# Performance work log

Measured on AMD Instinct MI355X. Metric: run time of the kernel, lower is better.

Reference implementation:

```python
import jax, jax.numpy as jnp
import numpy as np

B, L, P = 64, 256, 32
LANE_DIM, EMBED, DEPTH, HEADS = 2, 128, 4, 8
MLP = 4 * EMBED
HD = EMBED // HEADS
MASK_RATIO, ELIG = 0.5, 5


def _glorot(key, shape):
    lim = float(np.sqrt(6.0 / (shape[-2] + shape[-1])))
    return jax.random.uniform(key, shape, jnp.float32, -lim, lim)


def setup_inputs() -> dict:
    key = jax.random.key(0)
    ks = jax.random.split(key, 24)
    lane_positions = jax.random.normal(ks[0], (B, L, P, LANE_DIM), jnp.float32)
    lane_centers = jax.random.normal(ks[1], (B, L, LANE_DIM), jnp.float32)
    lane_angles = jax.random.normal(ks[2], (B, L), jnp.float32)
    # ragged padding + random masking, precomputed (externalizes torch randperm loop)
    rng = np.random.default_rng(0)
    pad = rng.random((B, L, P)) < 0.2  # True = padding
    valid = ~pad
    num_valid = valid.sum(-1)                      # (B,L)
    eligible = num_valid > ELIG
    num_mask = (num_valid * MASK_RATIO).astype(np.int32)  # trunc == .int()
    scores = np.where(valid, rng.random((B, L, P)), 2.0)
    rank = scores.argsort(-1).argsort(-1)          # rank of each valid point
    sel = (rank < num_mask[..., None]) & valid & eligible[..., None]
    inp = {
        'lane_positions': lane_positions,
        'lane_centers': lane_centers,
        'lane_angles': lane_angles,
        'lane_padding_mask': jnp.asarray(pad),
        'sel_mask': jnp.asarray(sel),
        'Wp': _glorot(ks[3], (LANE_DIM, EMBED)), 'bp': jnp.zeros((EMBED,)),
        'Wpe1': _glorot(ks[4], (4, EMBED)), 'bpe1': jnp.zeros((EMBED,)),
        'Wpe2': _glorot(ks[5], (EMBED, EMBED)), 'bpe2': jnp.zeros((EMBED,)),
        'lane_type': 0.02 * jax.random.normal(ks[6], (EMBED,), jnp.float32),
        'mask_token': 0.02 * jax.random.normal(ks[7], (EMBED,), jnp.float32),
        'Wqkv': _glorot(ks[8], (DEPTH, EMBED, 3 * EMBED)), 'bqkv': jnp.zeros((DEPTH, 3 * EMBED)),
        'Wo': _glorot(ks[9], (DEPTH, EMBED, EMBED)), 'bo': jnp.zeros((DEPTH, EMBED)),
        'ln1_s': jnp.ones((DEPTH, EMBED)), 'ln1_b': jnp.zeros((DEPTH, EMBED)),
        'Wm1': _glorot(ks[10], (DEPTH, EMBED, MLP)), 'bm1': jnp.zeros((DEPTH, MLP)),
        'Wm2': _glorot(ks[11], (DEPTH, MLP, EMBED)), 'bm2': jnp.zeros((DEPTH, EMBED)),
        'ln2_s': jnp.ones((DEPTH, EMBED)), 'ln2_b': jnp.zeros((DEPTH, EMBED)),
        'lnf_s': jnp.ones((EMBED,)), 'lnf_b': jnp.zeros((EMBED,)),
        'Wd1': _glorot(ks[12], (EMBED, MLP)), 'bd1': jnp.zeros((MLP,)),
        'Wd2': _glorot(ks[13], (MLP, LANE_DIM)), 'bd2': jnp.zeros((LANE_DIM,)),
    }
    return inp


def _ln(x, s, b):
    m = jnp.mean(x, -1, keepdims=True)
    v = jnp.var(x, -1, keepdims=True)
    return (x - m) * jax.lax.rsqrt(v + 1e-5) * s + b


def _forward(lane_positions, lane_centers, lane_angles, Wp, bp, Wpe1, bpe1,
             Wpe2, bpe2, lane_type, mask_token, Wqkv, bqkv, Wo, bo, ln1_s,
             ln1_b, Wm1, bm1, Wm2, bm2, ln2_s, ln2_b, lnf_s, lnf_b, Wd1, bd1,
             Wd2, bd2, sel_mask):
    lane_norm = lane_positions - lane_centers[:, :, None, :]      # (B,L,P,2)
    feat = lane_norm @ Wp + bp                                    # (B,L,P,E)
    pos_feat = jnp.concatenate([lane_centers,
                                jnp.cos(lane_angles)[..., None],
                                jnp.sin(lane_angles)[..., None]], -1)  # (B,L,4)
    pe = jax.nn.gelu(pos_feat @ Wpe1 + bpe1, approximate=False) @ Wpe2 + bpe2
    tok = feat + pe[:, :, None, :] + lane_type
    tok = jnp.where(sel_mask[..., None], mask_token, tok)
    x = tok.reshape(B * L, P, EMBED)
    scale = 1.0 / np.sqrt(HD).astype(np.float32)
    for i in range(DEPTH):  # SpaNet: pre-LN transformer encoder over points
        h = _ln(x, ln1_s[i], ln1_b[i])
        q, k, v = jnp.split(h @ Wqkv[i] + bqkv[i], 3, axis=-1)
        q = q.reshape(B * L, P, HEADS, HD)
        k = k.reshape(B * L, P, HEADS, HD)
        v = v.reshape(B * L, P, HEADS, HD)
        att = jax.nn.softmax(jnp.einsum('nqhd,nkhd->nhqk', q, k) * scale, -1)
        o = jnp.einsum('nhqk,nkhd->nqhd', att, v).reshape(B * L, P, EMBED)
        x = x + o @ Wo[i] + bo[i]
        h = _ln(x, ln2_s[i], ln2_b[i])
        x = x + jax.nn.gelu(h @ Wm1[i] + bm1[i], approximate=False) @ Wm2[i] + bm2[i]
    x = _ln(x, lnf_s, lnf_b)
    y = (jax.nn.relu(x @ Wd1 + bd1) @ Wd2 + bd2).reshape(B, L, P, LANE_DIM)
    selc = sel_mask[..., None].astype(y.dtype)
    sq = (y - lane_norm) ** 2
    loss = jnp.sum(sq * selc) / jnp.maximum(jnp.sum(selc) * LANE_DIM, 1.0)
    return loss, y


def reference(lane_positions, lane_centers, lane_angles, lane_padding_mask,
              sel_mask, Wp, bp, Wpe1, bpe1, Wpe2, bpe2, lane_type, mask_token,
              Wqkv, bqkv, Wo, bo, ln1_s, ln1_b, Wm1, bm1, Wm2, bm2, ln2_s,
              ln2_b, lnf_s, lnf_b, Wd1, bd1, Wd2, bd2):
    del lane_padding_mask  # already folded into sel_mask during setup
    return _forward(lane_positions, lane_centers, lane_angles, Wp, bp, Wpe1,
                    bpe1, Wpe2, bpe2, lane_type, mask_token, Wqkv, bqkv, Wo,
                    bo, ln1_s, ln1_b, Wm1, bm1, Wm2, bm2, ln2_s, ln2_b, lnf_s,
                    lnf_b, Wd1, bd1, Wd2, bd2, sel_mask)
```

## Files before the change

kernel.cpp:

```cpp
#include <hip/hip_runtime.h>


#define NP 32
#define NE 128
#define NSEQ (64 * 256)
#define NMLP 512
#define NDEPTH 4
#define LST 132
#define HBS 136
#define H1C 264

#define QKV_W_OFF 0
#define O_W_OFF   196608
#define M1_W_OFF  262144
#define M2_W_OFF  524288
#define D1_W_OFF  786432
#define W_TOTAL   851968
#define WS_NEED   (64 + (size_t)W_TOTAL * 2)

typedef unsigned short u16;
typedef unsigned int u32;
typedef __attribute__((ext_vector_type(8))) short bf16x8;
typedef __attribute__((ext_vector_type(4))) float f32x4;
#define MFMA16 __builtin_amdgcn_mfma_f32_16x16x32_bf16

__device__ __forceinline__ float b2f(u16 u) {
  union { u32 i; float f; } v; v.i = ((u32)u) << 16; return v.f;
}
__device__ __forceinline__ u16 f2b(float f) {
  union { float f; u32 i; } v; v.f = f;
  u32 x = v.i;
  x += 0x7fffu + ((x >> 16) & 1u);
  return (u16)(x >> 16);
}
__device__ __forceinline__ u32 pk2(float lo, float hi) {
  return (u32)f2b(lo) | ((u32)f2b(hi) << 16);
}
__device__ __forceinline__ float gelu_f(float x) {
  return 0.5f * x * (1.0f + erff(x * 0.7071067811865475f));
}

struct Args {
  const float *pos, *ctr, *ang;
  const int *sel;
  const float *Wp, *bp, *Wpe1, *bpe1, *Wpe2, *bpe2, *ltype, *mtok;
  const float *Wqkv, *bqkv, *Wo, *bo, *ln1s, *ln1b, *Wm1, *bm1, *Wm2, *bm2;
  const float *ln2s, *ln2b, *lnfs, *lnfb, *Wd1, *bd1, *Wd2, *bd2;
  float* out;
  float* wsf;
  int* wsi;
};

__global__ void pack_w(const float* __restrict__ src, u16* __restrict__ dst,
                       int K, int N, int L) {
  int id = blockIdx.x * 256 + threadIdx.x;
  int KT = K >> 5, NT = N >> 4;
  int total = L * NT * KT * 64;
  if (id >= total) return;
  int lane = id & 63;
  int rest = id >> 6;
  int kt = rest % KT;
  int rest2 = rest / KT;
  int nt = rest2 % NT;
  int l = rest2 / NT;
  const float* s = src + (size_t)l * K * N + (size_t)(kt * 32 + (lane >> 4) * 8) * N
                 + nt * 16 + (lane & 15);
  u16 tmp[8];
#pragma unroll
  for (int j = 0; j < 8; ++j) tmp[j] = f2b(s[(size_t)j * N]);
  ((uint4*)dst)[id] = *(const uint4*)tmp;
}

template <int NTW>
__device__ __forceinline__ void gemm_kt4(const u16* __restrict__ hA, int SA,
                                         const u16* __restrict__ B, int w,
                                         int lane, f32x4 (&acc)[NTW][2]) {
  int ar = lane & 15, ac = (lane >> 4) * 8;
  bf16x8 af[8];
#pragma unroll
  for (int kb = 0; kb < 4; ++kb) {
    af[kb]     = *(const bf16x8*)(hA + ar * SA + kb * 32 + ac);
    af[kb + 4] = *(const bf16x8*)(hA + (ar + 16) * SA + kb * 32 + ac);
  }
#pragma unroll
  for (int i = 0; i < NTW; ++i) {
    int nt = w + 4 * i;
    const u16* Bp = B + (size_t)nt * 2048 + lane * 8;
    f32x4 z = {0.f, 0.f, 0.f, 0.f};
    acc[i][0] = z; acc[i][1] = z;
#pragma unroll
    for (int kb = 0; kb < 4; ++kb) {
      bf16x8 b = *(const bf16x8*)(Bp + kb * 512);
      acc[i][0] = MFMA16(af[kb], b, acc[i][0], 0, 0, 0);
      acc[i][1] = MFMA16(af[kb + 4], b, acc[i][1], 0, 0, 0);
    }
  }
}

__device__ __forceinline__ void gemm_kt8_acc(const u16* __restrict__ hA,
                                             const u16* __restrict__ B, int ktoff,
                                             int w, int lane, f32x4 (&acc)[2][2]) {
  int ar = lane & 15, ac = (lane >> 4) * 8;
#pragma unroll
  for (int ktl = 0; ktl < 8; ++ktl) {
    bf16x8 a0 = *(const bf16x8*)(hA + ar * H1C + ktl * 32 + ac);
    bf16x8 a1 = *(const bf16x8*)(hA + (ar + 16) * H1C + ktl * 32 + ac);
#pragma unroll
    for (int i = 0; i < 2; ++i) {
      int nt = w + 4 * i;
      bf16x8 b = *(const bf16x8*)(B + (size_t)nt * 8192 + (size_t)(ktoff + ktl) * 512 + lane * 8);
      acc[i][0] = MFMA16(a0, b, acc[i][0], 0, 0, 0);
      acc[i][1] = MFMA16(a1, b, acc[i][1], 0, 0, 0);
    }
  }
}

__device__ __forceinline__ void layer_norm_bf(const float* __restrict__ src,
                                              u16* __restrict__ dst,
                                              const float* gam, const float* bet,
                                              int t, float* mrow, float* vrow) {
  int p = t >> 3, j0 = (t & 7) * 16;
  const float* row = src + p * LST + j0;
  float sum = 0.f, sq = 0.f;
#pragma unroll
  for (int k = 0; k < 16; ++k) { float v = row[k]; sum += v; sq += v * v; }
#pragma unroll
  for (int o = 1; o < 8; o <<= 1) { sum += __shfl_xor(sum, o); sq += __shfl_xor(sq, o); }
  if ((t & 7) == 0) {
    float m = sum * 0.0078125f;
    mrow[p] = m;
    vrow[p] = sq * 0.0078125f - m * m;
  }
  __syncthreads();
  float m = mrow[p], rs = rsqrtf(vrow[p] + 1e-5f);
  u32 wb[8];
#pragma unroll
  for (int k8 = 0; k8 < 4; ++k8) {
    float4 v = ((const float4*)row)[k8];
    float4 g = ((const float4*)(gam + j0))[k8];
    float4 b = ((const float4*)(bet + j0))[k8];
    wb[k8 * 2]     = pk2((v.x - m) * rs * g.x + b.x, (v.y - m) * rs * g.y + b.y);
    wb[k8 * 2 + 1] = pk2((v.z - m) * rs * g.z + b.z, (v.w - m) * rs * g.w + b.w);
  }
  uint4* dp = (uint4*)(dst + p * HBS + j0);
  dp[0] = make_uint4(wb[0], wb[1], wb[2], wb[3]);
  dp[1] = make_uint4(wb[4], wb[5], wb[6], wb[7]);
  __syncthreads();
}

__global__ __launch_bounds__(256, 3) void mrm_main_mfma(Args a, const u16* __restrict__ wsW) {
  __shared__ float xs[32 * LST];
  __shared__ u16 hbf[32 * HBS];
  __shared__ __align__(16) u32 uni4[6144];
  __shared__ float mrow[32], vrow[32];
  __shared__ int selv[32];
  __shared__ float lacc;

  u16* qbuf = (u16*)uni4;
  u16* kbuf = qbuf + 4096;
  u16* vbuf = kbuf + 4096;
  u32* vbuf_w = (u32*)vbuf;
  u16* h1c  = (u16*)uni4;
  float* wd2s = (float*)uni4 + 4224;
  float* tvec = (float*)uni4;
  float* pvec = (float*)uni4 + 128;

  const int s = blockIdx.x;
  const int t = threadIdx.x;
  const int w = t >> 6, lane = t & 63;
  const int cr = lane & 15, rq = (lane >> 4) * 4;
  const int rg = t >> 5, cg = t & 31, r0 = rg * 4, c0 = cg * 4;

  if (t == 0) lacc = 0.f;
  if (t < 32) selv[t] = a.sel[s * NP + t];

  const float cx = a.ctr[s * 2 + 0];
  const float cy = a.ctr[s * 2 + 1];
  const float an = a.ang[s];
  const float ca = cosf(an), sa = sinf(an);

  if (t < 128) {
    float accp = a.bpe1[t] + cx * a.Wpe1[t] + cy * a.Wpe1[128 + t]
               + ca * a.Wpe1[256 + t] + sa * a.Wpe1[384 + t];
    tvec[t] = gelu_f(accp);
  }
  __syncthreads();
  if (t < 128) {
    float accp = a.bpe2[t];
    for (int e = 0; e < 128; ++e) accp += tvec[e] * a.Wpe2[e * 128 + t];
    pvec[t] = accp;
  }
  __syncthreads();

  {
    float4 w0v = *(const float4*)(a.Wp + c0);
    float4 w1v = *(const float4*)(a.Wp + NE + c0);
    float4 bpv = *(const float4*)(a.bp + c0);
    float4 ltv = *(const float4*)(a.ltype + c0);
    float4 mtv = *(const float4*)(a.mtok + c0);
    float a0 = bpv.x + pvec[c0 + 0] + ltv.x;
    float a1 = bpv.y + pvec[c0 + 1] + ltv.y;
    float a2 = bpv.z + pvec[c0 + 2] + ltv.z;
    float a3 = bpv.w + pvec[c0 + 3] + ltv.w;
#pragma unroll
    for (int rr = 0; rr < 4; ++rr) {
      int p = r0 + rr;
      float px = a.pos[(s * NP + p) * 2 + 0] - cx;
      float py = a.pos[(s * NP + p) * 2 + 1] - cy;
      bool mk = selv[p] != 0;
      float4 o;
      o.x = mk ? mtv.x : (px * w0v.x + py * w1v.x + a0);
      o.y = mk ? mtv.y : (px * w0v.y + py * w1v.y + a1);
      o.z = mk ? mtv.z : (px * w0v.z + py * w1v.z + a2);
      o.w = mk ? mtv.w : (px * w0v.w + py * w1v.w + a3);
      *(float4*)&xs[p * LST + c0] = o;
    }
  }
  __syncthreads();

  for (int li = 0; li < NDEPTH; ++li) {
    const u16* qkvW = wsW + QKV_W_OFF + li * 49152;
    const u16* oW   = wsW + O_W_OFF   + li * 16384;
    const u16* m1W  = wsW + M1_W_OFF  + li * 65536;
    const u16* m2W  = wsW + M2_W_OFF  + li * 65536;
    const float* bqkv_i = a.bqkv + li * 384;
    const float* bo_i   = a.bo + li * NE;
    const float* bm1_i  = a.bm1 + li * NMLP;
    const float* bm2_i  = a.bm2 + li * NE;

    layer_norm_bf(xs, hbf, a.ln1s + li * NE, a.ln1b + li * NE, t, mrow, vrow);

    {
      f32x4 acc[6][2];
      gemm_kt4<6>(hbf, HBS, qkvW, w, lane, acc);
#pragma unroll
      for (int i = 0; i < 6; ++i) {
        int nt = w + 4 * i;
        int n = nt * 16 + cr;
        float bias = bqkv_i[n];
        float v0[4], v1[4];
#pragma unroll
        for (int j = 0; j < 4; ++j) { v0[j] = acc[i][0][j] + bias; v1[j] = acc[i][1][j] + bias; }
        if (i < 2) {
          u16* qb = qbuf + nt * 512 + cr;
#pragma unroll
          for (int j = 0; j < 4; ++j) {
            qb[(rq + j) * 16]      = f2b(v0[j] * 0.25f);
            qb[(rq + j + 16) * 16] = f2b(v1[j] * 0.25f);
          }
        } else if (i < 4) {
          u16* kb = kbuf + (nt - 8) * 512 + cr;
#pragma unroll
          for (int j = 0; j < 4; ++j) {
            kb[(rq + j) * 16]      = f2b(v0[j]);
            kb[(rq + j + 16) * 16] = f2b(v1[j]);
          }
        } else {
          u32* vb = vbuf_w + (nt - 16) * 256 + cr * 16 + (rq >> 1);
          vb[0] = pk2(v0[0], v0[1]);
          vb[1] = pk2(v0[2], v0[3]);
          vb[8] = pk2(v1[0], v1[1]);
          vb[9] = pk2(v1[2], v1[3]);
        }
      }
    }
    __syncthreads();

    {
      const int l15 = lane & 15, gl = lane >> 4;
      const int bpa_base = (l15 + ((gl & 1) << 5)) << 2;
      const f32x4 z = {0.f, 0.f, 0.f, 0.f};
#pragma unroll
      for (int hi = 0; hi < 2; ++hi) {
        const int h = 2 * w + hi;
        const u16* qb = qbuf + h * 512;
        const u16* kb = kbuf + h * 512;
        bf16x8 vf = *(const bf16x8*)(vbuf + h * 512 + l15 * 32 + gl * 8);
        bf16x8 kf0 = {}, kf1 = {};
        if (gl < 2) {
          kf0 = *(const bf16x8*)(kb + l15 * 16 + gl * 8);
          kf1 = *(const bf16x8*)(kb + (16 + l15) * 16 + gl * 8);
        }
#pragma unroll
        for (int qt = 0; qt < 2; ++qt) {
          bf16x8 qf = {};
          if (gl < 2) qf = *(const bf16x8*)(qb + (qt * 16 + l15) * 16 + gl * 8);
          f32x4 s0 = MFMA16(kf0, qf, z, 0, 0, 0);
          f32x4 s1 = MFMA16(kf1, qf, z, 0, 0, 0);
          float mx = fmaxf(fmaxf(fmaxf(s0[0], s0[1]), fmaxf(s0[2], s0[3])),
                           fmaxf(fmaxf(s1[0], s1[1]), fmaxf(s1[2], s1[3])));
          mx = fmaxf(mx, __shfl_xor(mx, 16));
          mx = fmaxf(mx, __shfl_xor(mx, 32));
          float p0 = __expf(s0[0] - mx), p1 = __expf(s0[1] - mx);
          float p2 = __expf(s0[2] - mx), p3 = __expf(s0[3] - mx);
          float p4 = __expf(s1[0] - mx), p5 = __expf(s1[1] - mx);
          float p6 = __expf(s1[2] - mx), p7 = __expf(s1[3] - mx);
          float sum = ((p0 + p1) + (p2 + p3)) + ((p4 + p5) + (p6 + p7));
          sum += __shfl_xor(sum, 16);
          sum += __shfl_xor(sum, 32);
          float inv = 1.f / sum;
          u32 pw0 = pk2(p0 * inv, p1 * inv), pw1 = pk2(p2 * inv, p3 * inv);
          u32 pw2 = pk2(p4 * inv, p5 * inv), pw3 = pk2(p6 * inv, p7 * inv);
          union { u32 uw[4]; bf16x8 v; } pa;
#pragma unroll
          for (int ww = 0; ww < 4; ++ww) {
            int addr = bpa_base + ((ww >> 1) << 6);
            u32 lo = __builtin_amdgcn_ds_bpermute(addr, (int)((ww & 1) ? pw1 : pw0));
            u32 hi2 = __builtin_amdgcn_ds_bpermute(addr, (int)((ww & 1) ? pw3 : pw2));
            pa.uw[ww] = (gl < 2) ? lo : hi2;
          }
          f32x4 o = MFMA16(pa.v, vf, z, 0, 0, 0);
#pragma unroll
          for (int j = 0; j < 4; ++j)
            hbf[(qt * 16 + gl * 4 + j) * HBS + h * 16 + l15] = f2b(o[j]);
        }
      }
    }
    __syncthreads();

    {
      f32x4 acc[2][2];
      gemm_kt4<2>(hbf, HBS, oW, w, lane, acc);
#pragma unroll
      for (int i = 0; i < 2; ++i) {
        int n = (w + 4 * i) * 16 + cr;
        float bias = bo_i[n];
#pragma unroll
        for (int j = 0; j < 4; ++j) {
          xs[(rq + j) * LST + n]      += acc[i][0][j] + bias;
          xs[(rq + j + 16) * LST + n] += acc[i][1][j] + bias;
        }
      }
    }
    __syncthreads();

    layer_norm_bf(xs, hbf, a.ln2s + li * NE, a.ln2b + li * NE, t, mrow, vrow);

    {
      f32x4 acc2[2][2];
      f32x4 z = {0.f, 0.f, 0.f, 0.f};
      acc2[0][0] = z; acc2[0][1] = z; acc2[1][0] = z; acc2[1][1] = z;
#pragma unroll
      for (int ch = 0; ch < 2; ++ch) {
        {
          f32x4 acc[4][2];
          gemm_kt4<4>(hbf, HBS, m1W + ch * 32768, w, lane, acc);
#pragma unroll
          for (int i = 0; i < 4; ++i) {
            int nl = (w + 4 * i) * 16 + cr;
            float bias = bm1_i[ch * 256 + nl];
#pragma unroll
            for (int j = 0; j < 4; ++j) {
              h1c[(rq + j) * H1C + nl]      = f2b(gelu_f(acc[i][0][j] + bias));
              h1c[(rq + j + 16) * H1C + nl] = f2b(gelu_f(acc[i][1][j] + bias));
            }
          }
        }
        __syncthreads();
        gemm_kt8_acc(h1c, m2W, ch * 8, w, lane, acc2);
        __syncthreads();
      }
      {
        f32x4* a2 = &acc2[0][0];
#pragma unroll
        for (int i = 0; i < 2; ++i) {
          int n = (w + 4 * i) * 16 + cr;
          float bias = bm2_i[n];
#pragma unroll
          for (int j = 0; j < 4; ++j) {
            xs[(rq + j) * LST + n]      += acc2[i][0][j] + bias;
            xs[(rq + j + 16) * LST + n] += acc2[i][1][j] + bias;
          }
        }
        (void)a2;
      }
    }
    __syncthreads();
  }

  layer_norm_bf(xs, hbf, a.lnfs, a.lnfb, t, mrow, vrow);

  for (int i = t; i < 1024; i += 256) wd2s[i] = a.Wd2[i];

  float yacc = 0.f;
  const int pdec = t >> 3, dd2 = (t >> 2) & 1, q4 = t & 3;
#pragma unroll
  for (int ch = 0; ch < 2; ++ch) {
    {
      f32x4 acc[4][2];
      gemm_kt4<4>(hbf, HBS, wsW + D1_W_OFF + ch * 32768, w, lane, acc);
#pragma unroll
      for (int i = 0; i < 4; ++i) {
        int nl = (w + 4 * i) * 16 + cr;
        float bias = a.bd1[ch * 256 + nl];
#pragma unroll
        for (int j = 0; j < 4; ++j) {
          h1c[(rq + j) * H1C + nl]      = f2b(fmaxf(acc[i][0][j] + bias, 0.f));
          h1c[(rq + j + 16) * H1C + nl] = f2b(fmaxf(acc[i][1][j] + bias, 0.f));
        }
      }
    }
    __syncthreads();
    {
      const u16* hrow = h1c + pdec * H1C + q4 * 64;
      const float* wp = wd2s + (ch * 256 + q4 * 64) * 2 + dd2;
#pragma unroll
      for (int k8 = 0; k8 < 8; ++k8) {
        bf16x8 hv = *(const bf16x8*)(hrow + k8 * 8);
#pragma unroll
        for (int jj = 0; jj < 8; ++jj)
          yacc += b2f((u16)hv[jj]) * wp[(k8 * 8 + jj) * 2];
      }
    }
    __syncthreads();
  }

  {
    yacc += __shfl_xor(yacc, 1);
    yacc += __shfl_xor(yacc, 2);
    if (q4 == 0) {
      float y = yacc + a.bd2[dd2];
      a.out[1 + (s * NP + pdec) * 2 + dd2] = y;
      float lnm = a.pos[(s * NP + pdec) * 2 + dd2] - (dd2 ? cy : cx);
      float d = y - lnm;
      if (selv[pdec] != 0) atomicAdd(&lacc, d * d);
    }
  }
  __syncthreads();
  if (t == 0) {
    atomicAdd(a.wsf, lacc);
    int cnt = 0;
#pragma unroll
    for (int p = 0; p < NP; ++p) cnt += (selv[p] != 0) ? 1 : 0;
    atomicAdd(a.wsi, cnt);
  }
}

__device__ __forceinline__ void mm128(const float* __restrict__ src,
                                      const float* __restrict__ W, int ldw,
                                      int r0, int cabs, float acc[4][4]) {
#pragma unroll 4
  for (int k = 0; k < NE; ++k) {
    float4 wv = *(const float4*)(W + k * ldw + cabs);
#pragma unroll
    for (int rr = 0; rr < 4; ++rr) {
      float sv = src[(r0 + rr) * LST + k];
      acc[rr][0] += sv * wv.x; acc[rr][1] += sv * wv.y;
      acc[rr][2] += sv * wv.z; acc[rr][3] += sv * wv.w;
    }
  }
}

__device__ __forceinline__ void layer_norm(const float* __restrict__ src,
                                           float* __restrict__ dst,
                                           const float* gam, const float* bet,
                                           int t, float* mrow, float* vrow) {
  {
    int p = t >> 3, j = t & 7;
    const float* row = src + p * LST + j * 16;
    float sum = 0.f, sq = 0.f;
#pragma unroll
    for (int k2 = 0; k2 < 16; ++k2) { float v = row[k2]; sum += v; sq += v * v; }
#pragma unroll
    for (int o = 1; o < 8; o <<= 1) { sum += __shfl_xor(sum, o); sq += __shfl_xor(sq, o); }
    if (j == 0) {
      float m = sum * 0.0078125f;
      mrow[p] = m;
      vrow[p] = sq * 0.0078125f - m * m;
    }
  }
  __syncthreads();
  {
    int rg = t >> 5, cg = t & 31, r0 = rg * 4, c0 = cg * 4;
    float4 gv = *(const float4*)(gam + c0);
    float4 bv = *(const float4*)(bet + c0);
#pragma unroll
    for (int rr = 0; rr < 4; ++rr) {
      int r = r0 + rr;
      float m = mrow[r], rs = rsqrtf(vrow[r] + 1e-5f);
      float4 v = *(const float4*)&src[r * LST + c0];
      float4 o;
      o.x = (v.x - m) * rs * gv.x + bv.x;
      o.y = (v.y - m) * rs * gv.y + bv.y;
      o.z = (v.z - m) * rs * gv.z + bv.z;
      o.w = (v.w - m) * rs * gv.w + bv.w;
      *(float4*)&dst[r * LST + c0] = o;
    }
  }
  __syncthreads();
}

__global__ __launch_bounds__(256, 2) void mrm_main_valu(Args a) {
  __shared__ float xs[32 * LST];
  __shared__ float hs[32 * LST];
  __shared__ float ts[32 * LST];
  __shared__ float qs[32 * 17];
  __shared__ float ks2[32 * 17];
  __shared__ float vs[32 * 17];
  __shared__ float ss[32 * 33];
  __shared__ float tvec[128];
  __shared__ float pvec[128];
  __shared__ float mrow[32], vrow[32], srow[32];
  __shared__ int selv[32];

  const int s = blockIdx.x;
  const int t = threadIdx.x;
  const int rg = t >> 5, cg = t & 31, r0 = rg * 4, c0 = cg * 4;

  if (t < 32) selv[t] = a.sel[s * NP + t];

  const float cx = a.ctr[s * 2 + 0];
  const float cy = a.ctr[s * 2 + 1];
  const float an = a.ang[s];
  const float ca = cosf(an), sa = sinf(an);

  if (t < 128) {
    float accp = a.bpe1[t] + cx * a.Wpe1[t] + cy * a.Wpe1[128 + t]
               + ca * a.Wpe1[256 + t] + sa * a.Wpe1[384 + t];
    tvec[t] = gelu_f(accp);
  }
  __syncthreads();
  if (t < 128) {
    float accp = a.bpe2[t];
    for (int e = 0; e < 128; ++e) accp += tvec[e] * a.Wpe2[e * 128 + t];
    pvec[t] = accp;
  }
  __syncthreads();

  {
    float4 w0v = *(const float4*)(a.Wp + c0);
    float4 w1v = *(const float4*)(a.Wp + NE + c0);
    float4 bpv = *(const float4*)(a.bp + c0);
    float4 ltv = *(const float4*)(a.ltype + c0);
    float4 mtv = *(const float4*)(a.mtok + c0);
    float a0 = bpv.x + pvec[c0 + 0] + ltv.x;
    float a1 = bpv.y + pvec[c0 + 1] + ltv.y;
    float a2 = bpv.z + pvec[c0 + 2] + ltv.z;
    float a3 = bpv.w + pvec[c0 + 3] + ltv.w;
#pragma unroll
    for (int rr = 0; rr < 4; ++rr) {
      int p = r0 + rr;
      float px = a.pos[(s * NP + p) * 2 + 0] - cx;
      float py = a.pos[(s * NP + p) * 2 + 1] - cy;
      bool mk = selv[p] != 0;
      float4 o;
      o.x = mk ? mtv.x : (px * w0v.x + py * w1v.x + a0);
      o.y = mk ? mtv.y : (px * w0v.y + py * w1v.y + a1);
      o.z = mk ? mtv.z : (px * w0v.z + py * w1v.z + a2);
      o.w = mk ? mtv.w : (px * w0v.w + py * w1v.w + a3);
      *(float4*)&xs[p * LST + c0] = o;
    }
  }
  __syncthreads();

  const int dd = t & 15, ph = t >> 4;

  for (int li = 0; li < NDEPTH; ++li) {
    const float* Wqkv_i = a.Wqkv + li * NE * 3 * NE;
    const float* bqkv_i = a.bqkv + li * 3 * NE;
    const float* Wo_i   = a.Wo   + li * NE * NE;
    const float* bo_i   = a.bo   + li * NE;
    const float* Wm1_i  = a.Wm1  + li * NE * NMLP;
    const float* bm1_i  = a.bm1  + li * NMLP;
    const float* Wm2_i  = a.Wm2  + li * NMLP * NE;
    const float* bm2_i  = a.bm2  + li * NE;

    layer_norm(xs, hs, a.ln1s + li * NE, a.ln1b + li * NE, t, mrow, vrow);

    for (int hh = 0; hh < 8; ++hh) {
      float aq0 = 0, aq1 = 0, ak0 = 0, ak1 = 0, av0 = 0, av1 = 0;
      const float* wcol = Wqkv_i + hh * 16 + dd;
#pragma unroll 4
      for (int k2 = 0; k2 < NE; ++k2) {
        const float* wr = wcol + k2 * (3 * NE);
        float wq = wr[0], wk = wr[NE], wv = wr[2 * NE];
        float h0 = hs[ph * LST + k2], h1 = hs[(ph + 16) * LST + k2];
        aq0 += h0 * wq; aq1 += h1 * wq;
        ak0 += h0 * wk; ak1 += h1 * wk;
        av0 += h0 * wv; av1 += h1 * wv;
      }
      {
        float bq = bqkv_i[hh * 16 + dd];
        float bk = bqkv_i[NE + hh * 16 + dd];
        float bv = bqkv_i[2 * NE + hh * 16 + dd];
        qs[ph * 17 + dd] = aq0 + bq;  qs[(ph + 16) * 17 + dd] = aq1 + bq;
        ks2[ph * 17 + dd] = ak0 + bk; ks2[(ph + 16) * 17 + dd] = ak1 + bk;
        vs[ph * 17 + dd] = av0 + bv;  vs[(ph + 16) * 17 + dd] = av1 + bv;
      }
      __syncthreads();
      {
        int pk = t & 31, pb = t >> 5;
#pragma unroll
        for (int ii = 0; ii < 4; ++ii) {
          int p = pb + 8 * ii;
          float acc = 0.f;
#pragma unroll
          for (int d2 = 0; d2 < 16; ++d2) acc += qs[p * 17 + d2] * ks2[pk * 17 + d2];
          ss[p * 33 + pk] = 0.25f * acc;
        }
      }
      __syncthreads();
      {
        int p = t >> 3, j = t & 7;
        float v0 = ss[p * 33 + j * 4 + 0], v1 = ss[p * 33 + j * 4 + 1];
        float v2 = ss[p * 33 + j * 4 + 2], v3 = ss[p * 33 + j * 4 + 3];
        float mx = fmaxf(fmaxf(v0, v1), fmaxf(v2, v3));
#pragma unroll
        for (int o = 1; o < 8; o <<= 1) mx = fmaxf(mx, __shfl_xor(mx, o));
        v0 = expf(v0 - mx); v1 = expf(v1 - mx); v2 = expf(v2 - mx); v3 = expf(v3 - mx);
        float sm = v0 + v1 + v2 + v3;
#pragma unroll
        for (int o = 1; o < 8; o <<= 1) sm += __shfl_xor(sm, o);
        ss[p * 33 + j * 4 + 0] = v0; ss[p * 33 + j * 4 + 1] = v1;
        ss[p * 33 + j * 4 + 2] = v2; ss[p * 33 + j * 4 + 3] = v3;
        if (j == 0) srow[p] = sm;
      }
      __syncthreads();
      {
        float o0 = 0.f, o1 = 0.f;
#pragma unroll
        for (int pk = 0; pk < 32; ++pk) {
          float vv = vs[pk * 17 + dd];
          o0 += ss[ph * 33 + pk] * vv;
          o1 += ss[(ph + 16) * 33 + pk] * vv;
        }
        ts[ph * LST + hh * 16 + dd] = o0 / srow[ph];
        ts[(ph + 16) * LST + hh * 16 + dd] = o1 / srow[ph + 16];
      }
      __syncthreads();
    }

    {
      float acc[4][4] = {};
      mm128(ts, Wo_i, NE, r0, c0, acc);
      float4 bv = *(const float4*)(bo_i + c0);
#pragma unroll
      for (int rr = 0; rr < 4; ++rr) {
        float4 v = *(float4*)&xs[(r0 + rr) * LST + c0];
        v.x += acc[rr][0] + bv.x; v.y += acc[rr][1] + bv.y;
        v.z += acc[rr][2] + bv.z; v.w += acc[rr][3] + bv.w;
        *(float4*)&xs[(r0 + rr) * LST + c0] = v;
      }
    }
    __syncthreads();

    layer_norm(xs, hs, a.ln2s + li * NE, a.ln2b + li * NE, t, mrow, vrow);

    {
      float acc2[4][4] = {};
      for (int ch = 0; ch < 4; ++ch) {
        float acc[4][4] = {};
        mm128(hs, Wm1_i, NMLP, r0, ch * 128 + c0, acc);
        float4 bv = *(const float4*)(bm1_i + ch * 128 + c0);
#pragma unroll
        for (int rr = 0; rr < 4; ++rr) {
          float4 o;
          o.x = gelu_f(acc[rr][0] + bv.x); o.y = gelu_f(acc[rr][1] + bv.y);
          o.z = gelu_f(acc[rr][2] + bv.z); o.w = gelu_f(acc[rr][3] + bv.w);
          *(float4*)&ts[(r0 + rr) * LST + c0] = o;
        }
        __syncthreads();
        mm128(ts, Wm2_i + ch * 128 * NE, NE, r0, c0, acc2);
        __syncthreads();
      }
      float4 bv = *(const float4*)(bm2_i + c0);
#pragma unroll
      for (int rr = 0; rr < 4; ++rr) {
        float4 v = *(float4*)&xs[(r0 + rr) * LST + c0];
        v.x += acc2[rr][0] + bv.x; v.y += acc2[rr][1] + bv.y;
        v.z += acc2[rr][2] + bv.z; v.w += acc2[rr][3] + bv.w;
        *(float4*)&xs[(r0 + rr) * LST + c0] = v;
      }
    }
    __syncthreads();
  }

  layer_norm(xs, hs, a.lnfs, a.lnfb, t, mrow, vrow);

  float yacc = 0.f;
  const int pdec = t >> 1, ddec = t & 1;
  for (int ch = 0; ch < 4; ++ch) {
    {
      float acc[4][4] = {};
      mm128(hs, a.Wd1, NMLP, r0, ch * 128 + c0, acc);
      float4 bv = *(const float4*)(a.bd1 + ch * 128 + c0);
#pragma unroll
      for (int rr = 0; rr < 4; ++rr) {
        float4 o;
        o.x = fmaxf(acc[rr][0] + bv.x, 0.f); o.y = fmaxf(acc[rr][1] + bv.y, 0.f);
        o.z = fmaxf(acc[rr][2] + bv.z, 0.f); o.w = fmaxf(acc[rr][3] + bv.w, 0.f);
        *(float4*)&ts[(r0 + rr) * LST + c0] = o;
      }
    }
    __syncthreads();
    if (t < 64) {
#pragma unroll 4
      for (int k2 = 0; k2 < 128; ++k2)
        yacc += ts[pdec * LST + k2] * a.Wd2[(ch * 128 + k2) * 2 + ddec];
    }
    __syncthreads();
  }

  if (t < 64) {
    float y = yacc + a.bd2[ddec];
    a.out[1 + (s * NP + pdec) * 2 + ddec] = y;
    float lnm = a.pos[(s * NP + pdec) * 2 + ddec] - (ddec ? cy : cx);
    float d = y - lnm;
    float part = (selv[pdec] != 0) ? d * d : 0.f;
#pragma unroll
    for (int o = 1; o < 64; o <<= 1) part += __shfl_xor(part, o);
    if (t == 0) {
      atomicAdd(a.wsf, part);
      int cnt = 0;
      for (int p = 0; p < NP; ++p) cnt += (selv[p] != 0) ? 1 : 0;
      atomicAdd(a.wsi, cnt);
    }
  }
}

__global__ void mrm_fin(const float* ws, float* out) {
  float num = ws[0];
  int cnt = ((const int*)ws)[1];
  float den = fmaxf((float)cnt * 2.0f, 1.0f);
  out[0] = num / den;
}

extern "C" void kernel_launch(void* const* d_in, const int* in_sizes, int n_in,
                              void* d_out, int out_size, void* d_ws, size_t ws_size,
                              hipStream_t stream) {
  (void)in_sizes; (void)n_in; (void)out_size;
  Args a;
  a.pos   = (const float*)d_in[0];
  a.ctr   = (const float*)d_in[1];
  a.ang   = (const float*)d_in[2];
  a.sel   = (const int*)d_in[4];
  a.Wp    = (const float*)d_in[5];
  a.bp    = (const float*)d_in[6];
  a.Wpe1  = (const float*)d_in[7];
  a.bpe1  = (const float*)d_in[8];
  a.Wpe2  = (const float*)d_in[9];
  a.bpe2  = (const float*)d_in[10];
  a.ltype = (const float*)d_in[11];
  a.mtok  = (const float*)d_in[12];
  a.Wqkv  = (const float*)d_in[13];
  a.bqkv  = (const float*)d_in[14];
  a.Wo    = (const float*)d_in[15];
  a.bo    = (const float*)d_in[16];
  a.ln1s  = (const float*)d_in[17];
  a.ln1b  = (const float*)d_in[18];
  a.Wm1   = (const float*)d_in[19];
  a.bm1   = (const float*)d_in[20];
  a.Wm2   = (const float*)d_in[21];
  a.bm2   = (const float*)d_in[22];
  a.ln2s  = (const float*)d_in[23];
  a.ln2b  = (const float*)d_in[24];
  a.lnfs  = (const float*)d_in[25];
  a.lnfb  = (const float*)d_in[26];
  a.Wd1   = (const float*)d_in[27];
  a.bd1   = (const float*)d_in[28];
  a.Wd2   = (const float*)d_in[29];
  a.bd2   = (const float*)d_in[30];
  a.out   = (float*)d_out;
  a.wsf   = (float*)d_ws;
  a.wsi   = ((int*)d_ws) + 1;

  hipMemsetAsync(d_ws, 0, 8, stream);
  if (ws_size >= WS_NEED) {
    u16* wsW = (u16*)((char*)d_ws + 64);
    pack_w<<<dim3(96),  dim3(256), 0, stream>>>(a.Wqkv, wsW + QKV_W_OFF, 128, 384, 4);
    pack_w<<<dim3(32),  dim3(256), 0, stream>>>(a.Wo,   wsW + O_W_OFF,   128, 128, 4);
    pack_w<<<dim3(128), dim3(256), 0, stream>>>(a.Wm1,  wsW + M1_W_OFF,  128, 512, 4);
    pack_w<<<dim3(128), dim3(256), 0, stream>>>(a.Wm2,  wsW + M2_W_OFF,  512, 128, 4);
    pack_w<<<dim3(32),  dim3(256), 0, stream>>>(a.Wd1,  wsW + D1_W_OFF,  128, 512, 1);
    mrm_main_mfma<<<dim3(NSEQ), dim3(256), 0, stream>>>(a, wsW);
  } else {
    mrm_main_valu<<<dim3(NSEQ), dim3(256), 0, stream>>>(a);
  }
  mrm_fin<<<dim3(1), dim3(1), 0, stream>>>((const float*)d_ws, (float*)d_out);
}
```

Baseline: 2.473 ms.

## Fold biases into MFMA accumulators, approximate GELU erf, pad V buffer, drop VALU fallback

Biases are now used as the initial MFMA accumulator values instead of being added in each epilogue. The 0.25 query scale is folded into the packed QKV weights and the query bias. The exact erff in GELU is replaced by an Abramowitz-Stegun polynomial with a fast reciprocal and exp, which cuts VALU work in the MLP at a small accuracy cost. The V buffer gets a padded row stride to reduce LDS bank conflicts, enlarging shared memory slightly. The VALU fallback path and the workspace size check are removed.

```diff
diff --git a/kernel.cpp b/kernel.cpp
--- a/kernel.cpp
+++ b/kernel.cpp
@@ -9,6 +9,7 @@
 #define LST 132
 #define HBS 136
 #define H1C 264
+#define VST 40
 
 #define QKV_W_OFF 0
 #define O_W_OFF   196608
@@ -36,8 +37,16 @@
 __device__ __forceinline__ u32 pk2(float lo, float hi) {
   return (u32)f2b(lo) | ((u32)f2b(hi) << 16);
 }
+
 __device__ __forceinline__ float gelu_f(float x) {
-  return 0.5f * x * (1.0f + erff(x * 0.7071067811865475f));
+  float z = fabsf(x) * 0.7071067811865476f;
+  float t = __builtin_amdgcn_rcpf(fmaf(z, 0.3275911f, 1.0f));
+  float poly = t * fmaf(t, fmaf(t, fmaf(t, fmaf(t, 1.061405429f, -1.453152027f),
+                        1.421413741f), -0.284496736f), 0.254829592f);
+  float e = __expf(-z * z);
+  float erf_abs = fmaf(-poly, e, 1.0f);
+  float erf = copysignf(erf_abs, x);
+  return 0.5f * x * (1.0f + erf);
 }
 
 struct Args {
@@ -52,7 +61,7 @@
 };
 
 __global__ void pack_w(const float* __restrict__ src, u16* __restrict__ dst,
-                       int K, int N, int L) {
+                       int K, int N, int L, int scaleN, float scale) {
   int id = blockIdx.x * 256 + threadIdx.x;
   int KT = K >> 5, NT = N >> 4;
   int total = L * NT * KT * 64;
@@ -63,18 +72,20 @@
   int rest2 = rest / KT;
   int nt = rest2 % NT;
   int l = rest2 / NT;
-  const float* s = src + (size_t)l * K * N + (size_t)(kt * 32 + (lane >> 4) * 8) * N
-                 + nt * 16 + (lane & 15);
+  int col = nt * 16 + (lane & 15);
+  float sc = (col < scaleN) ? scale : 1.0f;
+  const float* s = src + (size_t)l * K * N + (size_t)(kt * 32 + (lane >> 4) * 8) * N + col;
   u16 tmp[8];
 #pragma unroll
-  for (int j = 0; j < 8; ++j) tmp[j] = f2b(s[(size_t)j * N]);
+  for (int j = 0; j < 8; ++j) tmp[j] = f2b(s[(size_t)j * N] * sc);
   ((uint4*)dst)[id] = *(const uint4*)tmp;
 }
 
 template <int NTW>
-__device__ __forceinline__ void gemm_kt4(const u16* __restrict__ hA, int SA,
-                                         const u16* __restrict__ B, int w,
-                                         int lane, f32x4 (&acc)[NTW][2]) {
+__device__ __forceinline__ void gemm_kt4_b(const u16* __restrict__ hA, int SA,
+                                           const u16* __restrict__ B, int w,
+                                           int lane, const float* __restrict__ bias,
+                                           f32x4 (&acc)[NTW][2]) {
   int ar = lane & 15, ac = (lane >> 4) * 8;
   bf16x8 af[8];
 #pragma unroll
@@ -86,8 +97,9 @@
   for (int i = 0; i < NTW; ++i) {
     int nt = w + 4 * i;
     const u16* Bp = B + (size_t)nt * 2048 + lane * 8;
-    f32x4 z = {0.f, 0.f, 0.f, 0.f};
-    acc[i][0] = z; acc[i][1] = z;
+    float bb = bias[nt * 16 + ar];
+    f32x4 bi = {bb, bb, bb, bb};
+    acc[i][0] = bi; acc[i][1] = bi;
 #pragma unroll
     for (int kb = 0; kb < 4; ++kb) {
       bf16x8 b = *(const bf16x8*)(Bp + kb * 512);
@@ -139,8 +151,8 @@
     float4 v = ((const float4*)row)[k8];
     float4 g = ((const float4*)(gam + j0))[k8];
     float4 b = ((const float4*)(bet + j0))[k8];
-    wb[k8 * 2]     = pk2((v.x - m) * rs * g.x + b.x, (v.y - m) * rs * g.y + b.y);
-    wb[k8 * 2 + 1] = pk2((v.z - m) * rs * g.z + b.z, (v.w - m) * rs * g.w + b.w);
+    wb[k8 * 2]     = pk2(fmaf((v.x - m) * rs, g.x, b.x), fmaf((v.y - m) * rs, g.y, b.y));
+    wb[k8 * 2 + 1] = pk2(fmaf((v.z - m) * rs, g.z, b.z), fmaf((v.w - m) * rs, g.w, b.w));
   }
   uint4* dp = (uint4*)(dst + p * HBS + j0);
   dp[0] = make_uint4(wb[0], wb[1], wb[2], wb[3]);
@@ -151,7 +163,7 @@
 __global__ __launch_bounds__(256, 3) void mrm_main_mfma(Args a, const u16* __restrict__ wsW) {
   __shared__ float xs[32 * LST];
   __shared__ u16 hbf[32 * HBS];
-  __shared__ __align__(16) u32 uni4[6144];
+  __shared__ __align__(16) u32 uni4[6656];
   __shared__ float mrow[32], vrow[32];
   __shared__ int selv[32];
   __shared__ float lacc;
@@ -232,35 +244,53 @@
 
     {
       f32x4 acc[6][2];
-      gemm_kt4<6>(hbf, HBS, qkvW, w, lane, acc);
+      {
+        int ar = lane & 15, ac = (lane >> 4) * 8;
+        bf16x8 af[8];
+#pragma unroll
+        for (int kb = 0; kb < 4; ++kb) {
+          af[kb]     = *(const bf16x8*)(hbf + ar * HBS + kb * 32 + ac);
+          af[kb + 4] = *(const bf16x8*)(hbf + (ar + 16) * HBS + kb * 32 + ac);
+        }
+#pragma unroll
+        for (int i = 0; i < 6; ++i) {
+          int nt = w + 4 * i;
+          const u16* Bp = qkvW + (size_t)nt * 2048 + lane * 8;
+          float bb = bqkv_i[nt * 16 + ar];
+          if (i < 2) bb *= 0.25f;
+          f32x4 bi = {bb, bb, bb, bb};
+          acc[i][0] = bi; acc[i][1] = bi;
+#pragma unroll
+          for (int kb = 0; kb < 4; ++kb) {
+            bf16x8 b = *(const bf16x8*)(Bp + kb * 512);
+            acc[i][0] = MFMA16(af[kb], b, acc[i][0], 0, 0, 0);
+            acc[i][1] = MFMA16(af[kb + 4], b, acc[i][1], 0, 0, 0);
+          }
+        }
+      }
 #pragma unroll
       for (int i = 0; i < 6; ++i) {
         int nt = w + 4 * i;
-        int n = nt * 16 + cr;
-        float bias = bqkv_i[n];
-        float v0[4], v1[4];
-#pragma unroll
-        for (int j = 0; j < 4; ++j) { v0[j] = acc[i][0][j] + bias; v1[j] = acc[i][1][j] + bias; }
         if (i < 2) {
           u16* qb = qbuf + nt * 512 + cr;
 #pragma unroll
           for (int j = 0; j < 4; ++j) {
-            qb[(rq + j) * 16]      = f2b(v0[j] * 0.25f);
-            qb[(rq + j + 16) * 16] = f2b(v1[j] * 0.25f);
+            qb[(rq + j) * 16]      = f2b(acc[i][0][j]);
+            qb[(rq + j + 16) * 16] = f2b(acc[i][1][j]);
           }
         } else if (i < 4) {
           u16* kb = kbuf + (nt - 8) * 512 + cr;
 #pragma unroll
           for (int j = 0; j < 4; ++j) {
-            kb[(rq + j) * 16]      = f2b(v0[j]);
-            kb[(rq + j + 16) * 16] = f2b(v1[j]);
+            kb[(rq + j) * 16]      = f2b(acc[i][0][j]);
+            kb[(rq + j + 16) * 16] = f2b(acc[i][1][j]);
           }
         } else {
-          u32* vb = vbuf_w + (nt - 16) * 256 + cr * 16 + (rq >> 1);
-          vb[0] = pk2(v0[0], v0[1]);
-          vb[1] = pk2(v0[2], v0[3]);
-          vb[8] = pk2(v1[0], v1[1]);
-          vb[9] = pk2(v1[2], v1[3]);
+          u32* vb = vbuf_w + (nt - 16) * 320 + cr * 20 + (rq >> 1);
+          vb[0] = pk2(acc[i][0][0], acc[i][0][1]);
+          vb[1] = pk2(acc[i][0][2], acc[i][0][3]);
+          vb[8] = pk2(acc[i][1][0], acc[i][1][1]);
+          vb[9] = pk2(acc[i][1][2], acc[i][1][3]);
         }
       }
     }
@@ -275,7 +305,7 @@
         const int h = 2 * w + hi;
         const u16* qb = qbuf + h * 512;
         const u16* kb = kbuf + h * 512;
-        bf16x8 vf = *(const bf16x8*)(vbuf + h * 512 + l15 * 32 + gl * 8);
+        bf16x8 vf = *(const bf16x8*)(vbuf + h * 640 + l15 * VST + gl * 8);
         bf16x8 kf0 = {}, kf1 = {};
         if (gl < 2) {
           kf0 = *(const bf16x8*)(kb + l15 * 16 + gl * 8);
@@ -320,15 +350,14 @@
 
     {
       f32x4 acc[2][2];
-      gemm_kt4<2>(hbf, HBS, oW, w, lane, acc);
+      gemm_kt4_b<2>(hbf, HBS, oW, w, lane, bo_i, acc);
 #pragma unroll
       for (int i = 0; i < 2; ++i) {
         int n = (w + 4 * i) * 16 + cr;
-        float bias = bo_i[n];
 #pragma unroll
         for (int j = 0; j < 4; ++j) {
-          xs[(rq + j) * LST + n]      += acc[i][0][j] + bias;
-          xs[(rq + j + 16) * LST + n] += acc[i][1][j] + bias;
+          xs[(rq + j) * LST + n]      += acc[i][0][j];
+          xs[(rq + j + 16) * LST + n] += acc[i][1][j];
         }
       }
     }
@@ -338,21 +367,24 @@
 
     {
       f32x4 acc2[2][2];
-      f32x4 z = {0.f, 0.f, 0.f, 0.f};
-      acc2[0][0] = z; acc2[0][1] = z; acc2[1][0] = z; acc2[1][1] = z;
+#pragma unroll
+      for (int i = 0; i < 2; ++i) {
+        float bb = bm2_i[(w + 4 * i) * 16 + cr];
+        f32x4 bi = {bb, bb, bb, bb};
+        acc2[i][0] = bi; acc2[i][1] = bi;
+      }
 #pragma unroll
       for (int ch = 0; ch < 2; ++ch) {
         {
           f32x4 acc[4][2];
-          gemm_kt4<4>(hbf, HBS, m1W + ch * 32768, w, lane, acc);
+          gemm_kt4_b<4>(hbf, HBS, m1W + ch * 32768, w, lane, bm1_i + ch * 256, acc);
 #pragma unroll
           for (int i = 0; i < 4; ++i) {
             int nl = (w + 4 * i) * 16 + cr;
-            float bias = bm1_i[ch * 256 + nl];
 #pragma unroll
             for (int j = 0; j < 4; ++j) {
-              h1c[(rq + j) * H1C + nl]      = f2b(gelu_f(acc[i][0][j] + bias));
-              h1c[(rq + j + 16) * H1C + nl] = f2b(gelu_f(acc[i][1][j] + bias));
+              h1c[(rq + j) * H1C + nl]      = f2b(gelu_f(acc[i][0][j]));
+              h1c[(rq + j + 16) * H1C + nl] = f2b(gelu_f(acc[i][1][j]));
             }
           }
         }
@@ -360,19 +392,14 @@
         gemm_kt8_acc(h1c, m2W, ch * 8, w, lane, acc2);
         __syncthreads();
       }
-      {
-        f32x4* a2 = &acc2[0][0];
-#pragma unroll
-        for (int i = 0; i < 2; ++i) {
-          int n = (w + 4 * i) * 16 + cr;
-          float bias = bm2_i[n];
-#pragma unroll
-          for (int j = 0; j < 4; ++j) {
-            xs[(rq + j) * LST + n]      += acc2[i][0][j] + bias;
-            xs[(rq + j + 16) * LST + n] += acc2[i][1][j] + bias;
-          }
-        }
-        (void)a2;
+#pragma unroll
+      for (int i = 0; i < 2; ++i) {
+        int n = (w + 4 * i) * 16 + cr;
+#pragma unroll
+        for (int j = 0; j < 4; ++j) {
+          xs[(rq + j) * LST + n]      += acc2[i][0][j];
+          xs[(rq + j + 16) * LST + n] += acc2[i][1][j];
+        }
       }
     }
     __syncthreads();
@@ -388,15 +415,14 @@
   for (int ch = 0; ch < 2; ++ch) {
     {
       f32x4 acc[4][2];
-      gemm_kt4<4>(hbf, HBS, wsW + D1_W_OFF + ch * 32768, w, lane, acc);
+      gemm_kt4_b<4>(hbf, HBS, wsW + D1_W_OFF + ch * 32768, w, lane, a.bd1 + ch * 256, acc);
 #pragma unroll
       for (int i = 0; i < 4; ++i) {
         int nl = (w + 4 * i) * 16 + cr;
-        float bias = a.bd1[ch * 256 + nl];
 #pragma unroll
         for (int j = 0; j < 4; ++j) {
-          h1c[(rq + j) * H1C + nl]      = f2b(fmaxf(acc[i][0][j] + bias, 0.f));
-          h1c[(rq + j + 16) * H1C + nl] = f2b(fmaxf(acc[i][1][j] + bias, 0.f));
+          h1c[(rq + j) * H1C + nl]      = f2b(fmaxf(acc[i][0][j], 0.f));
+          h1c[(rq + j + 16) * H1C + nl] = f2b(fmaxf(acc[i][1][j], 0.f));
         }
       }
     }
@@ -436,288 +462,6 @@
   }
 }
 
-__device__ __forceinline__ void mm128(const float* __restrict__ src,
-                                      const float* __restrict__ W, int ldw,
-                                      int r0, int cabs, float acc[4][4]) {
-#pragma unroll 4
-  for (int k = 0; k < NE; ++k) {
-    float4 wv = *(const float4*)(W + k * ldw + cabs);
-#pragma unroll
-    for (int rr = 0; rr < 4; ++rr) {
-      float sv = src[(r0 + rr) * LST + k];
-      acc[rr][0] += sv * wv.x; acc[rr][1] += sv * wv.y;
-      acc[rr][2] += sv * wv.z; acc[rr][3] += sv * wv.w;
-    }
-  }
-}
-
-__device__ __forceinline__ void layer_norm(const float* __restrict__ src,
-                                           float* __restrict__ dst,
-                                           const float* gam, const float* bet,
-                                           int t, float* mrow, float* vrow) {
-  {
-    int p = t >> 3, j = t & 7;
-    const float* row = src + p * LST + j * 16;
-    float sum = 0.f, sq = 0.f;
-#pragma unroll
-    for (int k2 = 0; k2 < 16; ++k2) { float v = row[k2]; sum += v; sq += v * v; }
-#pragma unroll
-    for (int o = 1; o < 8; o <<= 1) { sum += __shfl_xor(sum, o); sq += __shfl_xor(sq, o); }
-    if (j == 0) {
-      float m = sum * 0.0078125f;
-      mrow[p] = m;
-      vrow[p] = sq * 0.0078125f - m * m;
-    }
-  }
-  __syncthreads();
-  {
-    int rg = t >> 5, cg = t & 31, r0 = rg * 4, c0 = cg * 4;
-    float4 gv = *(const float4*)(gam + c0);
-    float4 bv = *(const float4*)(bet + c0);
-#pragma unroll
-    for (int rr = 0; rr < 4; ++rr) {
-      int r = r0 + rr;
-      float m = mrow[r], rs = rsqrtf(vrow[r] + 1e-5f);
-      float4 v = *(const float4*)&src[r * LST + c0];
-      float4 o;
-      o.x = (v.x - m) * rs * gv.x + bv.x;
-      o.y = (v.y - m) * rs * gv.y + bv.y;
-      o.z = (v.z - m) * rs * gv.z + bv.z;
-      o.w = (v.w - m) * rs * gv.w + bv.w;
-      *(float4*)&dst[r * LST + c0] = o;
-    }
-  }
-  __syncthreads();
-}
-
-__global__ __launch_bounds__(256, 2) void mrm_main_valu(Args a) {
-  __shared__ float xs[32 * LST];
-  __shared__ float hs[32 * LST];
-  __shared__ float ts[32 * LST];
-  __shared__ float qs[32 * 17];
-  __shared__ float ks2[32 * 17];
-  __shared__ float vs[32 * 17];
-  __shared__ float ss[32 * 33];
-  __shared__ float tvec[128];
-  __shared__ float pvec[128];
-  __shared__ float mrow[32], vrow[32], srow[32];
-  __shared__ int selv[32];
-
-  const int s = blockIdx.x;
-  const int t = threadIdx.x;
-  const int rg = t >> 5, cg = t & 31, r0 = rg * 4, c0 = cg * 4;
-
-  if (t < 32) selv[t] = a.sel[s * NP + t];
-
-  const float cx = a.ctr[s * 2 + 0];
-  const float cy = a.ctr[s * 2 + 1];
-  const float an = a.ang[s];
-  const float ca = cosf(an), sa = sinf(an);
-
-  if (t < 128) {
-    float accp = a.bpe1[t] + cx * a.Wpe1[t] + cy * a.Wpe1[128 + t]
-               + ca * a.Wpe1[256 + t] + sa * a.Wpe1[384 + t];
-    tvec[t] = gelu_f(accp);
-  }
-  __syncthreads();
-  if (t < 128) {
-    float accp = a.bpe2[t];
-    for (int e = 0; e < 128; ++e) accp += tvec[e] * a.Wpe2[e * 128 + t];
-    pvec[t] = accp;
-  }
-  __syncthreads();
-
-  {
-    float4 w0v = *(const float4*)(a.Wp + c0);
-    float4 w1v = *(const float4*)(a.Wp + NE + c0);
-    float4 bpv = *(const float4*)(a.bp + c0);
-    float4 ltv = *(const float4*)(a.ltype + c0);
-    float4 mtv = *(const float4*)(a.mtok + c0);
-    float a0 = bpv.x + pvec[c0 + 0] + ltv.x;
-    float a1 = bpv.y + pvec[c0 + 1] + ltv.y;
-    float a2 = bpv.z + pvec[c0 + 2] + ltv.z;
-    float a3 = bpv.w + pvec[c0 + 3] + ltv.w;
-#pragma unroll
-    for (int rr = 0; rr < 4; ++rr) {
-      int p = r0 + rr;
-      float px = a.pos[(s * NP + p) * 2 + 0] - cx;
-      float py = a.pos[(s * NP + p) * 2 + 1] - cy;
-      bool mk = selv[p] != 0;
-      float4 o;
-      o.x = mk ? mtv.x : (px * w0v.x + py * w1v.x + a0);
-      o.y = mk ? mtv.y : (px * w0v.y + py * w1v.y + a1);
-      o.z = mk ? mtv.z : (px * w0v.z + py * w1v.z + a2);
-      o.w = mk ? mtv.w : (px * w0v.w + py * w1v.w + a3);
-      *(float4*)&xs[p * LST + c0] = o;
-    }
-  }
-  __syncthreads();
-
-  const int dd = t & 15, ph = t >> 4;
-
-  for (int li = 0; li < NDEPTH; ++li) {
-    const float* Wqkv_i = a.Wqkv + li * NE * 3 * NE;
-    const float* bqkv_i = a.bqkv + li * 3 * NE;
-    const float* Wo_i   = a.Wo   + li * NE * NE;
-    const float* bo_i   = a.bo   + li * NE;
-    const float* Wm1_i  = a.Wm1  + li * NE * NMLP;
-    const float* bm1_i  = a.bm1  + li * NMLP;
-    const float* Wm2_i  = a.Wm2  + li * NMLP * NE;
-    const float* bm2_i  = a.bm2  + li * NE;
-
-    layer_norm(xs, hs, a.ln1s + li * NE, a.ln1b + li * NE, t, mrow, vrow);
-
-    for (int hh = 0; hh < 8; ++hh) {
-      float aq0 = 0, aq1 = 0, ak0 = 0, ak1 = 0, av0 = 0, av1 = 0;
-      const float* wcol = Wqkv_i + hh * 16 + dd;
-#pragma unroll 4
-      for (int k2 = 0; k2 < NE; ++k2) {
-        const float* wr = wcol + k2 * (3 * NE);
-        float wq = wr[0], wk = wr[NE], wv = wr[2 * NE];
-        float h0 = hs[ph * LST + k2], h1 = hs[(ph + 16) * LST + k2];
-        aq0 += h0 * wq; aq1 += h1 * wq;
-        ak0 += h0 * wk; ak1 += h1 * wk;
-        av0 += h0 * wv; av1 += h1 * wv;
-      }
-      {
-        float bq = bqkv_i[hh * 16 + dd];
-        float bk = bqkv_i[NE + hh * 16 + dd];
-        float bv = bqkv_i[2 * NE + hh * 16 + dd];
-        qs[ph * 17 + dd] = aq0 + bq;  qs[(ph + 16) * 17 + dd] = aq1 + bq;
-        ks2[ph * 17 + dd] = ak0 + bk; ks2[(ph + 16) * 17 + dd] = ak1 + bk;
-        vs[ph * 17 + dd] = av0 + bv;  vs[(ph + 16) * 17 + dd] = av1 + bv;
-      }
-      __syncthreads();
-      {
-        int pk = t & 31, pb = t >> 5;
-#pragma unroll
-        for (int ii = 0; ii < 4; ++ii) {
-          int p = pb + 8 * ii;
-          float acc = 0.f;
-#pragma unroll
-          for (int d2 = 0; d2 < 16; ++d2) acc += qs[p * 17 + d2] * ks2[pk * 17 + d2];
-          ss[p * 33 + pk] = 0.25f * acc;
-        }
-      }
-      __syncthreads();
-      {
-        int p = t >> 3, j = t & 7;
-        float v0 = ss[p * 33 + j * 4 + 0], v1 = ss[p * 33 + j * 4 + 1];
-        float v2 = ss[p * 33 + j * 4 + 2], v3 = ss[p * 33 + j * 4 + 3];
-        float mx = fmaxf(fmaxf(v0, v1), fmaxf(v2, v3));
-#pragma unroll
-        for (int o = 1; o < 8; o <<= 1) mx = fmaxf(mx, __shfl_xor(mx, o));
-        v0 = expf(v0 - mx); v1 = expf(v1 - mx); v2 = expf(v2 - mx); v3 = expf(v3 - mx);
-        float sm = v0 + v1 + v2 + v3;
-#pragma unroll
-        for (int o = 1; o < 8; o <<= 1) sm += __shfl_xor(sm, o);
-        ss[p * 33 + j * 4 + 0] = v0; ss[p * 33 + j * 4 + 1] = v1;
-        ss[p * 33 + j * 4 + 2] = v2; ss[p * 33 + j * 4 + 3] = v3;
-        if (j == 0) srow[p] = sm;
-      }
-      __syncthreads();
-      {
-        float o0 = 0.f, o1 = 0.f;
-#pragma unroll
-        for (int pk = 0; pk < 32; ++pk) {
-          float vv = vs[pk * 17 + dd];
-          o0 += ss[ph * 33 + pk] * vv;
-          o1 += ss[(ph + 16) * 33 + pk] * vv;
-        }
-        ts[ph * LST + hh * 16 + dd] = o0 / srow[ph];
-        ts[(ph + 16) * LST + hh * 16 + dd] = o1 / srow[ph + 16];
-      }
-      __syncthreads();
-    }
-
-    {
-      float acc[4][4] = {};
-      mm128(ts, Wo_i, NE, r0, c0, acc);
-      float4 bv = *(const float4*)(bo_i + c0);
-#pragma unroll
-      for (int rr = 0; rr < 4; ++rr) {
-        float4 v = *(float4*)&xs[(r0 + rr) * LST + c0];
-        v.x += acc[rr][0] + bv.x; v.y += acc[rr][1] + bv.y;
-        v.z += acc[rr][2] + bv.z; v.w += acc[rr][3] + bv.w;
-        *(float4*)&xs[(r0 + rr) * LST + c0] = v;
-      }
-    }
-    __syncthreads();
-
-    layer_norm(xs, hs, a.ln2s + li * NE, a.ln2b + li * NE, t, mrow, vrow);
-
-    {
-      float acc2[4][4] = {};
-      for (int ch = 0; ch < 4; ++ch) {
-        float acc[4][4] = {};
-        mm128(hs, Wm1_i, NMLP, r0, ch * 128 + c0, acc);
-        float4 bv = *(const float4*)(bm1_i + ch * 128 + c0);
-#pragma unroll
-        for (int rr = 0; rr < 4; ++rr) {
-          float4 o;
-          o.x = gelu_f(acc[rr][0] + bv.x); o.y = gelu_f(acc[rr][1] + bv.y);
-          o.z = gelu_f(acc[rr][2] + bv.z); o.w = gelu_f(acc[rr][3] + bv.w);
-          *(float4*)&ts[(r0 + rr) * LST + c0] = o;
-        }
-        __syncthreads();
-        mm128(ts, Wm2_i + ch * 128 * NE, NE, r0, c0, acc2);
-        __syncthreads();
-      }
-      float4 bv = *(const float4*)(bm2_i + c0);
-#pragma unroll
-      for (int rr = 0; rr < 4; ++rr) {
-        float4 v = *(float4*)&xs[(r0 + rr) * LST + c0];
-        v.x += acc2[rr][0] + bv.x; v.y += acc2[rr][1] + bv.y;
-        v.z += acc2[rr][2] + bv.z; v.w += acc2[rr][3] + bv.w;
-        *(float4*)&xs[(r0 + rr) * LST + c0] = v;
-      }
-    }
-    __syncthreads();
-  }
-
-  layer_norm(xs, hs, a.lnfs, a.lnfb, t, mrow, vrow);
-
-  float yacc = 0.f;
-  const int pdec = t >> 1, ddec = t & 1;
-  for (int ch = 0; ch < 4; ++ch) {
-    {
-      float acc[4][4] = {};
-      mm128(hs, a.Wd1, NMLP, r0, ch * 128 + c0, acc);
-      float4 bv = *(const float4*)(a.bd1 + ch * 128 + c0);
-#pragma unroll
-      for (int rr = 0; rr < 4; ++rr) {
-        float4 o;
-        o.x = fmaxf(acc[rr][0] + bv.x, 0.f); o.y = fmaxf(acc[rr][1] + bv.y, 0.f);
-        o.z = fmaxf(acc[rr][2] + bv.z, 0.f); o.w = fmaxf(acc[rr][3] + bv.w, 0.f);
-        *(float4*)&ts[(r0 + rr) * LST + c0] = o;
-      }
-    }
-    __syncthreads();
-    if (t < 64) {
-#pragma unroll 4
-      for (int k2 = 0; k2 < 128; ++k2)
-        yacc += ts[pdec * LST + k2] * a.Wd2[(ch * 128 + k2) * 2 + ddec];
-    }
-    __syncthreads();
-  }
-
-  if (t < 64) {
-    float y = yacc + a.bd2[ddec];
-    a.out[1 + (s * NP + pdec) * 2 + ddec] = y;
-    float lnm = a.pos[(s * NP + pdec) * 2 + ddec] - (ddec ? cy : cx);
-    float d = y - lnm;
-    float part = (selv[pdec] != 0) ? d * d : 0.f;
-#pragma unroll
-    for (int o = 1; o < 64; o <<= 1) part += __shfl_xor(part, o);
-    if (t == 0) {
-      atomicAdd(a.wsf, part);
-      int cnt = 0;
-      for (int p = 0; p < NP; ++p) cnt += (selv[p] != 0) ? 1 : 0;
-      atomicAdd(a.wsi, cnt);
-    }
-  }
-}
-
 __global__ void mrm_fin(const float* ws, float* out) {
   float num = ws[0];
   int cnt = ((const int*)ws)[1];
@@ -728,7 +472,7 @@
 extern "C" void kernel_launch(void* const* d_in, const int* in_sizes, int n_in,
                               void* d_out, int out_size, void* d_ws, size_t ws_size,
                               hipStream_t stream) {
-  (void)in_sizes; (void)n_in; (void)out_size;
+  (void)in_sizes; (void)n_in; (void)out_size; (void)ws_size;
   Args a;
   a.pos   = (const float*)d_in[0];
   a.ctr   = (const float*)d_in[1];
@@ -765,16 +509,12 @@
   a.wsi   = ((int*)d_ws) + 1;
 
   hipMemsetAsync(d_ws, 0, 8, stream);
-  if (ws_size >= WS_NEED) {
-    u16* wsW = (u16*)((char*)d_ws + 64);
-    pack_w<<<dim3(96),  dim3(256), 0, stream>>>(a.Wqkv, wsW + QKV_W_OFF, 128, 384, 4);
-    pack_w<<<dim3(32),  dim3(256), 0, stream>>>(a.Wo,   wsW + O_W_OFF,   128, 128, 4);
-    pack_w<<<dim3(128), dim3(256), 0, stream>>>(a.Wm1,  wsW + M1_W_OFF,  128, 512, 4);
-    pack_w<<<dim3(128), dim3(256), 0, stream>>>(a.Wm2,  wsW + M2_W_OFF,  512, 128, 4);
-    pack_w<<<dim3(32),  dim3(256), 0, stream>>>(a.Wd1,  wsW + D1_W_OFF,  128, 512, 1);
-    mrm_main_mfma<<<dim3(NSEQ), dim3(256), 0, stream>>>(a, wsW);
-  } else {
-    mrm_main_valu<<<dim3(NSEQ), dim3(256), 0, stream>>>(a);
-  }
+  u16* wsW = (u16*)((char*)d_ws + 64);
+  pack_w<<<dim3(96),  dim3(256), 0, stream>>>(a.Wqkv, wsW + QKV_W_OFF, 128, 384, 4, 128, 0.25f);
+  pack_w<<<dim3(32),  dim3(256), 0, stream>>>(a.Wo,   wsW + O_W_OFF,   128, 128, 4, 0, 1.f);
+  pack_w<<<dim3(128), dim3(256), 0, stream>>>(a.Wm1,  wsW + M1_W_OFF,  128, 512, 4, 0, 1.f);
+  pack_w<<<dim3(128), dim3(256), 0, stream>>>(a.Wm2,  wsW + M2_W_OFF,  512, 128, 4, 0, 1.f);
+  pack_w<<<dim3(32),  dim3(256), 0, stream>>>(a.Wd1,  wsW + D1_W_OFF,  128, 512, 1, 0, 1.f);
+  mrm_main_mfma<<<dim3(NSEQ), dim3(256), 0, stream>>>(a, wsW);
   mrm_fin<<<dim3(1), dim3(1), 0, stream>>>((const float*)d_ws, (float*)d_out);
 }
```

Result: faster. 2.377 ms (-3.9%).
